# Kernel tuning notes

Measured on AMD Instinct MI355X. Metric: run time of the kernel, lower is better.

## Reference

```python
import jax, jax.numpy as jnp
import numpy as np

B, S, E = 2, 2048, 2048
H, KV, HD = 16, 4, 128  # num_heads, num_kv_heads, head_dim
G = H // KV             # query heads per kv head
ROPE_BASE = 10000.0


def rope_tables(dim, maxlen):
    freqs = 1.0 / ROPE_BASE ** (jnp.arange(0, dim, 2, dtype=jnp.float32) / dim)
    t = jnp.arange(maxlen, dtype=jnp.float32)
    f = jnp.outer(t, freqs)  # (maxlen, dim//2)
    return jnp.cos(f), jnp.sin(f)


def apply_rope(x, cos, sin):
    # x: (..., seq, heads, head_dim); interleaved-pair rotation
    s_len = x.shape[-3]
    c = cos[:s_len][:, None, :]
    s = sin[:s_len][:, None, :]
    x1 = x[..., ::2]
    x2 = x[..., 1::2]
    return jnp.stack([x1 * c - x2 * s, x1 * s + x2 * c], axis=-1).reshape(x.shape)


def setup_inputs() -> dict:
    key = jax.random.key(0)
    kx, kq, kk, kv, ko = jax.random.split(key, 5)
    x = jax.random.normal(kx, (B, S, E), dtype=jnp.float32)
    Wq = jax.random.normal(kq, (E, H * HD), dtype=jnp.float32) * 0.02
    Wk = jax.random.normal(kk, (E, KV * HD), dtype=jnp.float32) * 0.02
    Wv = jax.random.normal(kv, (E, KV * HD), dtype=jnp.float32) * 0.02
    Wo = jax.random.normal(ko, (H * HD, E), dtype=jnp.float32) * 0.02
    mask = jnp.tril(jnp.ones((S, S), dtype=bool))[None, None]  # causal (1,1,S,S)
    return {"x": x, "Wq": Wq, "Wk": Wk, "Wv": Wv, "Wo": Wo, "mask": mask}


def reference(x, Wq, Wk, Wv, Wo, mask):
    b, s, _ = x.shape
    cos, sin = rope_tables(HD, s)
    q = (x @ Wq).reshape(b, s, H, HD)
    k = (x @ Wk).reshape(b, s, KV, HD)
    v = (x @ Wv).reshape(b, s, KV, HD)
    q = apply_rope(q, cos, sin)
    k = apply_rope(k, cos, sin)
    if G > 1:
        k = jnp.repeat(k, G, axis=2)  # (b, s, H, HD)
        v = jnp.repeat(v, G, axis=2)
    q = jnp.transpose(q, (0, 2, 1, 3))  # (b, H, s, HD)
    k = jnp.transpose(k, (0, 2, 1, 3))
    v = jnp.transpose(v, (0, 2, 1, 3))
    scale = jnp.sqrt(jnp.float32(HD)).astype(q.dtype)
    scores = jnp.einsum("bhqd,bhkd->bhqk", q, k) / scale
    scores = jnp.where(mask, scores, jnp.finfo(scores.dtype).min)
    attn = jax.nn.softmax(scores, axis=-1)
    out = jnp.einsum("bhqk,bhkd->bhqd", attn, v)
    out = jnp.transpose(out, (0, 2, 1, 3)).reshape(b, s, H * HD)
    return out @ Wo
```

## Files before the change

kernel.cpp:

```cpp
#include <hip/hip_runtime.h>
#include <hip/hip_bf16.h>
#include <cstdint>

#define B_ 2
#define S_ 2048
#define E_ 2048
#define H_ 16
#define KV_ 4
#define HD_ 128
#define BS_ (B_*S_)
#define QKV_LD 3072
#define SM_SCALE 0.08838834764831845f
#define SC_LOG2E 0.1275424488538497f

typedef __attribute__((ext_vector_type(8))) __bf16 bf16x8;
typedef __attribute__((ext_vector_type(4))) float  floatx4;

__device__ __forceinline__ unsigned short f2bf(float f) {
  union { float f; unsigned u; } v; v.f = f;
  unsigned r = v.u + 0x7fffu + ((v.u >> 16) & 1u);
  return (unsigned short)(r >> 16);
}
__device__ __forceinline__ float bf2f(unsigned short u) {
  union { unsigned u; float f; } v; v.u = ((unsigned)u) << 16; return v.f;
}
__device__ __forceinline__ unsigned pack_bf16x2(float a, float b) {
  union { __hip_bfloat162 h; unsigned u; } v;
  v.h = __float22bfloat162_rn(make_float2(a, b));
  return v.u;
}

__device__ __forceinline__ void async_cp16(const void* g, void* l) {
  __builtin_amdgcn_global_load_lds(
      (const __attribute__((address_space(1))) void*)g,
      (__attribute__((address_space(3))) void*)l, 16, 0, 0);
}

__global__ __launch_bounds__(256)
void cvt_bf16(const float* __restrict__ src, unsigned short* __restrict__ dst,
              int n4) {
  int idx = blockIdx.x * 256 + threadIdx.x;
  if (idx >= n4) return;
  float4 v = *(const float4*)(src + (size_t)idx * 4);
  ushort4 o;
  o.x = f2bf(v.x); o.y = f2bf(v.y); o.z = f2bf(v.z); o.w = f2bf(v.w);
  *(ushort4*)(dst + (size_t)idx * 4) = o;
}

__global__ __launch_bounds__(256)
void cvt_bf16_t(const float* __restrict__ src, unsigned short* __restrict__ dst,
                int N, int dld, int noff) {
  __shared__ float tile[64 * 65];
  const int t = threadIdx.x;
  const int bk = blockIdx.y * 64, bn = blockIdx.x * 64;
  const int r = t >> 2, cg = t & 3;
#pragma unroll
  for (int i = 0; i < 4; ++i) {
    int c = cg * 16 + i * 4;
    float4 v = *(const float4*)(src + (size_t)(bk + r) * N + bn + c);
    tile[r * 65 + c] = v.x; tile[r * 65 + c + 1] = v.y;
    tile[r * 65 + c + 2] = v.z; tile[r * 65 + c + 3] = v.w;
  }
  __syncthreads();
  const int nl = t >> 2, kg = t & 3;
  union { unsigned short u[16]; uint4 q[2]; } o;
#pragma unroll
  for (int j = 0; j < 16; ++j)
    o.u[j] = f2bf(tile[(kg * 16 + j) * 65 + nl]);
  unsigned short* dp = dst + (size_t)(noff + bn + nl) * dld + bk + kg * 16;
  *(uint4*)(dp) = o.q[0];
  *(uint4*)(dp + 8) = o.q[1];
}

__global__ __launch_bounds__(256)
void rope_kernel(unsigned short* __restrict__ qkv) {
  const int PPR = 1280;
  int idx = blockIdx.x * 256 + threadIdx.x;
  if (idx >= BS_ * PPR) return;
  int row = idx / PPR, p = idx - row * PPR;
  int col = (p < 1024) ? (2 * p) : (2048 + 2 * (p - 1024));
  int d = p & 63;
  int s = row & (S_ - 1);
  float freq = expf(-(float)d * 0.14391156831212787f);
  float ang = (float)s * freq;
  float c = cosf(ang), sn = sinf(ang);
  unsigned short* ptr = qkv + (size_t)row * QKV_LD + col;
  float x1 = bf2f(ptr[0]), x2 = bf2f(ptr[1]);
  ptr[0] = f2bf(x1 * c - x2 * sn);
  ptr[1] = f2bf(x1 * sn + x2 * c);
}

__global__ __launch_bounds__(256)
void vtrans_kernel(const unsigned short* __restrict__ qkv,
                   unsigned short* __restrict__ vt) {
  __shared__ unsigned short tile[64 * 72];
  const int tid = threadIdx.x;
  const int s0 = blockIdx.x * 64;
  const int g = blockIdx.y >> 1;
  const int hh = (blockIdx.y & 1) * 64;
  const int b = g >> 2, kvh = g & 3;
#pragma unroll
  for (int i = 0; i < 2; ++i) {
    int chunk = tid + i * 256;
    int r = chunk >> 3, c = (chunk & 7) * 8;
    uint4 v = *(const uint4*)(qkv + (size_t)(b * S_ + s0 + r) * QKV_LD + 2560 + kvh * HD_ + hh + c);
    *(uint4*)(tile + r * 72 + c) = v;
  }
  __syncthreads();
#pragma unroll
  for (int i = 0; i < 2; ++i) {
    int chunk = tid + i * 256;
    int hdr = chunk >> 3, sc = (chunk & 7) * 8;
    union { unsigned short u[8]; uint4 v; } t;
#pragma unroll
    for (int j = 0; j < 8; ++j) t.u[j] = tile[(sc + j) * 72 + hdr];
    *(uint4*)(vt + (size_t)(g * HD_ + hh + hdr) * S_ + s0 + sc) = t.v;
  }
}

template<bool OUT_BF16>
__global__ __launch_bounds__(256, 2)
void gemm_tn(const unsigned short* __restrict__ A,
             const unsigned short* __restrict__ BT,
             void* __restrict__ C, int M, int N, int K) {
  __shared__ unsigned short Ash[128 * 32];
  __shared__ unsigned short Bsh[128 * 32];
  const int tid = threadIdx.x;
  const int l = tid & 63;
  const int l16 = l & 15, l4 = l >> 4;
  const int wave = tid >> 6;
  const int wm = (wave >> 1) * 64, wn = (wave & 1) * 64;
  const int bm = blockIdx.y * 128, bn = blockIdx.x * 128;

  const int srow = l >> 2;
  const int sg = (((l & 3) - (l >> 4)) & 3) * 8;

  floatx4 acc[4][4] = {};

  for (int kb = 0; kb < K; kb += 32) {
    __syncthreads();
#pragma unroll
    for (int i = 0; i < 2; ++i) {
      int cc = wave + i * 4;
      async_cp16(A + (size_t)(bm + 16 * cc + srow) * K + kb + sg, &Ash[cc * 512]);
      async_cp16(BT + (size_t)(bn + 16 * cc + srow) * K + kb + sg, &Bsh[cc * 512]);
    }
    __syncthreads();
    bf16x8 af[4], bf[4];
#pragma unroll
    for (int t = 0; t < 4; ++t) {
      int row = wm + t * 16 + l16;
      int s = (l4 + (l16 >> 2)) & 3;
      af[t] = *(const bf16x8*)(Ash + row * 32 + s * 8);
    }
#pragma unroll
    for (int t = 0; t < 4; ++t) {
      int row = wn + t * 16 + l16;
      int s = (l4 + (l16 >> 2)) & 3;
      bf[t] = *(const bf16x8*)(Bsh + row * 32 + s * 8);
    }
#pragma unroll
    for (int tm = 0; tm < 4; ++tm)
#pragma unroll
      for (int tn = 0; tn < 4; ++tn)
        acc[tm][tn] = __builtin_amdgcn_mfma_f32_16x16x32_bf16(af[tm], bf[tn], acc[tm][tn], 0, 0, 0);
  }
#pragma unroll
  for (int tm = 0; tm < 4; ++tm)
#pragma unroll
    for (int tn = 0; tn < 4; ++tn)
#pragma unroll
      for (int r = 0; r < 4; ++r) {
        int row = bm + wm + tm * 16 + l4 * 4 + r;
        int col = bn + wn + tn * 16 + l16;
        float v = acc[tm][tn][r];
        if (OUT_BF16) ((unsigned short*)C)[(size_t)row * N + col] = f2bf(v);
        else          ((float*)C)[(size_t)row * N + col] = v;
      }
}

__global__ __launch_bounds__(256, 4)
void gqa_attention(const unsigned short* __restrict__ qkv,
                   const unsigned short* __restrict__ vt,
                   unsigned short* __restrict__ out) {
  __shared__ unsigned short Ksh[2][32 * 128];
  __shared__ unsigned short Vsh[2][128 * 32];

  const int tid = threadIdx.x, l = tid & 63, wave = tid >> 6;
  const int l16 = l & 15, l4 = l >> 4;
  const int g = blockIdx.x, b = g >> 2, kvh = g & 3;
  const int h = kvh * 4 + wave;

  const int k_subrow = l >> 4;
  const int v_subrow = l >> 2;
  const int gv = (((l & 3) - (l >> 4)) & 3) * 8;

  const int t = 127 - (int)blockIdx.y;
  const int qt = t * 16;
  const int nch = (qt >> 5) + 1;

  bf16x8 qf[4];
  {
    const unsigned short* qp = qkv + (size_t)(b * S_ + qt + l16) * QKV_LD + h * HD_;
#pragma unroll
    for (int c = 0; c < 4; ++c)
      qf[c] = *(const bf16x8*)(qp + c * 32 + l4 * 8);
  }
  asm volatile("s_waitcnt vmcnt(0)" ::: "memory");

  const unsigned short* kp[2];
  const unsigned short* vp[2];
#pragma unroll
  for (int i = 0; i < 2; ++i) {
    int cc = wave + i * 4;
    int krow = 4 * cc + k_subrow;
    int gk = (((l & 15) - krow) & 15) * 8;
    kp[i] = qkv + (size_t)(b * S_ + krow) * QKV_LD + 2048 + kvh * HD_ + gk;
    vp[i] = vt + (size_t)(g * HD_ + 16 * cc + v_subrow) * S_ + gv;
  }

#pragma unroll
  for (int i = 0; i < 2; ++i) {
    int cc = wave + i * 4;
    async_cp16(kp[i], &Ksh[0][cc * 512]);
    async_cp16(vp[i], &Vsh[0][cc * 512]);
  }

  float lsum = 0.f;
  floatx4 acc[8] = {};

  for (int it = 0; it < nch; ++it) {
    const int kb = it * 32;
    const int cur = it & 1;
    asm volatile("s_barrier" ::: "memory");
    {
      const int kb2 = (it + 1 < nch) ? kb + 32 : 0;
      const int ko = kb2 * QKV_LD;
#pragma unroll
      for (int i = 0; i < 2; ++i) {
        int cc = wave + i * 4;
        async_cp16(kp[i] + ko, &Ksh[cur ^ 1][cc * 512]);
        async_cp16(vp[i] + kb2, &Vsh[cur ^ 1][cc * 512]);
      }
    }
    asm volatile("s_waitcnt vmcnt(4)\n\ts_barrier" ::: "memory");

    floatx4 sacc[2] = {};
    __builtin_amdgcn_s_setprio(1);
#pragma unroll
    for (int half = 0; half < 2; ++half) {
      int krow = half * 16 + l16;
#pragma unroll
      for (int c = 0; c < 4; ++c) {
        int s = (c * 4 + l4 + l16) & 15;
        bf16x8 kf = *(const bf16x8*)(&Ksh[cur][krow * 128 + s * 8]);
        sacc[half] = __builtin_amdgcn_mfma_f32_16x16x32_bf16(kf, qf[c], sacc[half], 0, 0, 0);
      }
    }
    __builtin_amdgcn_s_setprio(0);

    float p[8];
    const bool need_mask = (kb + 31 > qt);
#pragma unroll
    for (int half = 0; half < 2; ++half)
#pragma unroll
      for (int r = 0; r < 4; ++r) {
        float v = fminf(sacc[half][r] * SC_LOG2E, 80.f);
        if (need_mask) {
          int ka = kb + half * 16 + l4 * 4 + r;
          if (ka > qt + l16) v = -3e38f;
        }
        float e = exp2f(v);
        p[half * 4 + r] = e;
        lsum += e;
      }

    unsigned u0 = pack_bf16x2(p[0], p[1]);
    unsigned u1 = pack_bf16x2(p[2], p[3]);
    unsigned u2 = pack_bf16x2(p[4], p[5]);
    unsigned u3 = pack_bf16x2(p[6], p[7]);
    asm("v_permlane32_swap_b32 %0, %1" : "+v"(u0), "+v"(u2));
    asm("v_permlane16_swap_b32 %0, %1" : "+v"(u0), "+v"(u2));
    asm("v_permlane32_swap_b32 %0, %1" : "+v"(u1), "+v"(u3));
    asm("v_permlane16_swap_b32 %0, %1" : "+v"(u1), "+v"(u3));
    union { unsigned w[4]; bf16x8 v8; } pun;
    pun.w[0] = u0; pun.w[1] = u1; pun.w[2] = u2; pun.w[3] = u3;
    const bf16x8 pf = pun.v8;

    __builtin_amdgcn_s_setprio(1);
#pragma unroll
    for (int u = 0; u < 8; ++u) {
      int row = u * 16 + l16;
      int s = (l4 + (l16 >> 2)) & 3;
      bf16x8 vf = *(const bf16x8*)(&Vsh[cur][row * 32 + s * 8]);
      acc[u] = __builtin_amdgcn_mfma_f32_16x16x32_bf16(vf, pf, acc[u], 0, 0, 0);
    }
    __builtin_amdgcn_s_setprio(0);
  }

  lsum += __shfl_xor(lsum, 16, 64);
  lsum += __shfl_xor(lsum, 32, 64);
  float inv = 1.0f / lsum;
  unsigned short* op = out + (size_t)(b * S_ + qt + l16) * 2048 + h * HD_;
#pragma unroll
  for (int u = 0; u < 8; ++u) {
    uint2 o;
    o.x = pack_bf16x2(acc[u][0] * inv, acc[u][1] * inv);
    o.y = pack_bf16x2(acc[u][2] * inv, acc[u][3] * inv);
    *(uint2*)(op + u * 16 + l4 * 4) = o;
  }
}

extern "C" void kernel_launch(void* const* d_in, const int* in_sizes, int n_in,
                              void* d_out, int out_size, void* d_ws, size_t ws_size,
                              hipStream_t stream) {
  const float* x  = (const float*)d_in[0];
  const float* Wq = (const float*)d_in[1];
  const float* Wk = (const float*)d_in[2];
  const float* Wv = (const float*)d_in[3];
  const float* Wo = (const float*)d_in[4];
  float* out = (float*)d_out;

  char* ws = (char*)d_ws;
  unsigned short* xb    = (unsigned short*)(ws);
  unsigned short* wqkvT = (unsigned short*)(ws + 16777216);
  unsigned short* woT   = (unsigned short*)(ws + 29360128);
  unsigned short* qkv   = (unsigned short*)(ws + 37748736);
  unsigned short* attn  = (unsigned short*)(ws + 62914560);
  unsigned short* vt    = (unsigned short*)(ws);

  cvt_bf16<<<(4096 * 2048 / 4 + 255) / 256, 256, 0, stream>>>(x, xb, 4096 * 2048 / 4);
  cvt_bf16_t<<<dim3(32, 32), 256, 0, stream>>>(Wq, wqkvT, 2048, 2048, 0);
  cvt_bf16_t<<<dim3(8, 32),  256, 0, stream>>>(Wk, wqkvT, 512,  2048, 2048);
  cvt_bf16_t<<<dim3(8, 32),  256, 0, stream>>>(Wv, wqkvT, 512,  2048, 2560);
  cvt_bf16_t<<<dim3(32, 32), 256, 0, stream>>>(Wo, woT,  2048, 2048, 0);

  gemm_tn<true><<<dim3(24, 32), 256, 0, stream>>>(xb, wqkvT, qkv, 4096, 3072, 2048);
  rope_kernel<<<(4096 * 1280 + 255) / 256, 256, 0, stream>>>(qkv);
  vtrans_kernel<<<dim3(32, 16), 256, 0, stream>>>(qkv, vt);
  gqa_attention<<<dim3(8, 128), 256, 0, stream>>>(qkv, vt, attn);
  gemm_tn<false><<<dim3(16, 32), 256, 0, stream>>>(attn, woT, out, 4096, 2048, 2048);
}
```

Measured before the change: 338.9 us.

## Process two 16-row query tiles per wave in attention to reuse K/V tiles

Each attention block now covers 32 query rows instead of 16, and each wave holds two query fragment sets that share every K and V shared-memory tile load. The grid halves along the query axis and the causal mask is applied only on the last chunk, using fixed per-tile conditions. This halves the K/V global and LDS traffic per query row. In exchange, register use roughly doubles from the two accumulator sets, so launch bounds drop to 2 blocks per CU, and there are fewer blocks to balance the causal workload.

```diff
diff --git a/kernel.cpp b/kernel.cpp
--- a/kernel.cpp
+++ b/kernel.cpp
@@ -179,7 +179,7 @@
       }
 }
 
-__global__ __launch_bounds__(256, 4)
+__global__ __launch_bounds__(256, 2)
 void gqa_attention(const unsigned short* __restrict__ qkv,
                    const unsigned short* __restrict__ vt,
                    unsigned short* __restrict__ out) {
@@ -195,16 +195,19 @@
   const int v_subrow = l >> 2;
   const int gv = (((l & 3) - (l >> 4)) & 3) * 8;
 
-  const int t = 127 - (int)blockIdx.y;
-  const int qt = t * 16;
-  const int nch = (qt >> 5) + 1;
-
-  bf16x8 qf[4];
+  const int t = 63 - (int)blockIdx.y;
+  const int qt = t * 32;
+  const int nch = t + 1;
+
+  bf16x8 qfA[4], qfB[4];
   {
-    const unsigned short* qp = qkv + (size_t)(b * S_ + qt + l16) * QKV_LD + h * HD_;
-#pragma unroll
-    for (int c = 0; c < 4; ++c)
-      qf[c] = *(const bf16x8*)(qp + c * 32 + l4 * 8);
+    const unsigned short* qpA = qkv + (size_t)(b * S_ + qt + l16) * QKV_LD + h * HD_;
+    const unsigned short* qpB = qpA + (size_t)16 * QKV_LD;
+#pragma unroll
+    for (int c = 0; c < 4; ++c) {
+      qfA[c] = *(const bf16x8*)(qpA + c * 32 + l4 * 8);
+      qfB[c] = *(const bf16x8*)(qpB + c * 32 + l4 * 8);
+    }
   }
   asm volatile("s_waitcnt vmcnt(0)" ::: "memory");
 
@@ -226,15 +229,14 @@
     async_cp16(vp[i], &Vsh[0][cc * 512]);
   }
 
-  float lsum = 0.f;
-  floatx4 acc[8] = {};
+  float lsumA = 0.f, lsumB = 0.f;
+  floatx4 accA[8] = {}, accB[8] = {};
 
   for (int it = 0; it < nch; ++it) {
-    const int kb = it * 32;
     const int cur = it & 1;
     asm volatile("s_barrier" ::: "memory");
     {
-      const int kb2 = (it + 1 < nch) ? kb + 32 : 0;
+      const int kb2 = (it + 1 < nch) ? (it + 1) * 32 : 0;
       const int ko = kb2 * QKV_LD;
 #pragma unroll
       for (int i = 0; i < 2; ++i) {
@@ -245,7 +247,7 @@
     }
     asm volatile("s_waitcnt vmcnt(4)\n\ts_barrier" ::: "memory");
 
-    floatx4 sacc[2] = {};
+    floatx4 saccA[2] = {}, saccB[2] = {};
     __builtin_amdgcn_s_setprio(1);
 #pragma unroll
     for (int half = 0; half < 2; ++half) {
@@ -254,38 +256,61 @@
       for (int c = 0; c < 4; ++c) {
         int s = (c * 4 + l4 + l16) & 15;
         bf16x8 kf = *(const bf16x8*)(&Ksh[cur][krow * 128 + s * 8]);
-        sacc[half] = __builtin_amdgcn_mfma_f32_16x16x32_bf16(kf, qf[c], sacc[half], 0, 0, 0);
+        saccA[half] = __builtin_amdgcn_mfma_f32_16x16x32_bf16(kf, qfA[c], saccA[half], 0, 0, 0);
+        saccB[half] = __builtin_amdgcn_mfma_f32_16x16x32_bf16(kf, qfB[c], saccB[half], 0, 0, 0);
       }
     }
     __builtin_amdgcn_s_setprio(0);
 
-    float p[8];
-    const bool need_mask = (kb + 31 > qt);
-#pragma unroll
-    for (int half = 0; half < 2; ++half)
-#pragma unroll
-      for (int r = 0; r < 4; ++r) {
-        float v = fminf(sacc[half][r] * SC_LOG2E, 80.f);
-        if (need_mask) {
-          int ka = kb + half * 16 + l4 * 4 + r;
-          if (ka > qt + l16) v = -3e38f;
+    float pA[8], pB[8];
+    if (it == nch - 1) {
+#pragma unroll
+      for (int half = 0; half < 2; ++half)
+#pragma unroll
+        for (int r = 0; r < 4; ++r) {
+          int kk = half * 16 + l4 * 4 + r;
+          float vA = fminf(saccA[half][r] * SC_LOG2E, 80.f);
+          if (kk > l16) vA = -3e38f;
+          float eA = exp2f(vA);
+          pA[half * 4 + r] = eA; lsumA += eA;
+          float vB = fminf(saccB[half][r] * SC_LOG2E, 80.f);
+          if (half == 1 && (l4 * 4 + r) > l16) vB = -3e38f;
+          float eB = exp2f(vB);
+          pB[half * 4 + r] = eB; lsumB += eB;
         }
-        float e = exp2f(v);
-        p[half * 4 + r] = e;
-        lsum += e;
-      }
-
-    unsigned u0 = pack_bf16x2(p[0], p[1]);
-    unsigned u1 = pack_bf16x2(p[2], p[3]);
-    unsigned u2 = pack_bf16x2(p[4], p[5]);
-    unsigned u3 = pack_bf16x2(p[6], p[7]);
-    asm("v_permlane32_swap_b32 %0, %1" : "+v"(u0), "+v"(u2));
-    asm("v_permlane16_swap_b32 %0, %1" : "+v"(u0), "+v"(u2));
-    asm("v_permlane32_swap_b32 %0, %1" : "+v"(u1), "+v"(u3));
-    asm("v_permlane16_swap_b32 %0, %1" : "+v"(u1), "+v"(u3));
-    union { unsigned w[4]; bf16x8 v8; } pun;
-    pun.w[0] = u0; pun.w[1] = u1; pun.w[2] = u2; pun.w[3] = u3;
-    const bf16x8 pf = pun.v8;
+    } else {
+#pragma unroll
+      for (int half = 0; half < 2; ++half)
+#pragma unroll
+        for (int r = 0; r < 4; ++r) {
+          float eA = exp2f(fminf(saccA[half][r] * SC_LOG2E, 80.f));
+          pA[half * 4 + r] = eA; lsumA += eA;
+          float eB = exp2f(fminf(saccB[half][r] * SC_LOG2E, 80.f));
+          pB[half * 4 + r] = eB; lsumB += eB;
+        }
+    }
+
+    unsigned a0 = pack_bf16x2(pA[0], pA[1]);
+    unsigned a1 = pack_bf16x2(pA[2], pA[3]);
+    unsigned a2 = pack_bf16x2(pA[4], pA[5]);
+    unsigned a3 = pack_bf16x2(pA[6], pA[7]);
+    asm("v_permlane32_swap_b32 %0, %1" : "+v"(a0), "+v"(a2));
+    asm("v_permlane16_swap_b32 %0, %1" : "+v"(a0), "+v"(a2));
+    asm("v_permlane32_swap_b32 %0, %1" : "+v"(a1), "+v"(a3));
+    asm("v_permlane16_swap_b32 %0, %1" : "+v"(a1), "+v"(a3));
+    unsigned b0 = pack_bf16x2(pB[0], pB[1]);
+    unsigned b1 = pack_bf16x2(pB[2], pB[3]);
+    unsigned b2 = pack_bf16x2(pB[4], pB[5]);
+    unsigned b3 = pack_bf16x2(pB[6], pB[7]);
+    asm("v_permlane32_swap_b32 %0, %1" : "+v"(b0), "+v"(b2));
+    asm("v_permlane16_swap_b32 %0, %1" : "+v"(b0), "+v"(b2));
+    asm("v_permlane32_swap_b32 %0, %1" : "+v"(b1), "+v"(b3));
+    asm("v_permlane16_swap_b32 %0, %1" : "+v"(b1), "+v"(b3));
+    union { unsigned w[4]; bf16x8 v8; } punA, punB;
+    punA.w[0] = a0; punA.w[1] = a1; punA.w[2] = a2; punA.w[3] = a3;
+    punB.w[0] = b0; punB.w[1] = b1; punB.w[2] = b2; punB.w[3] = b3;
+    const bf16x8 pfA = punA.v8;
+    const bf16x8 pfB = punB.v8;
 
     __builtin_amdgcn_s_setprio(1);
 #pragma unroll
@@ -293,21 +318,29 @@
       int row = u * 16 + l16;
       int s = (l4 + (l16 >> 2)) & 3;
       bf16x8 vf = *(const bf16x8*)(&Vsh[cur][row * 32 + s * 8]);
-      acc[u] = __builtin_amdgcn_mfma_f32_16x16x32_bf16(vf, pf, acc[u], 0, 0, 0);
+      accA[u] = __builtin_amdgcn_mfma_f32_16x16x32_bf16(vf, pfA, accA[u], 0, 0, 0);
+      accB[u] = __builtin_amdgcn_mfma_f32_16x16x32_bf16(vf, pfB, accB[u], 0, 0, 0);
     }
     __builtin_amdgcn_s_setprio(0);
   }
 
-  lsum += __shfl_xor(lsum, 16, 64);
-  lsum += __shfl_xor(lsum, 32, 64);
-  float inv = 1.0f / lsum;
-  unsigned short* op = out + (size_t)(b * S_ + qt + l16) * 2048 + h * HD_;
+  lsumA += __shfl_xor(lsumA, 16, 64);
+  lsumA += __shfl_xor(lsumA, 32, 64);
+  lsumB += __shfl_xor(lsumB, 16, 64);
+  lsumB += __shfl_xor(lsumB, 32, 64);
+  float invA = 1.0f / lsumA;
+  float invB = 1.0f / lsumB;
+  unsigned short* opA = out + (size_t)(b * S_ + qt + l16) * 2048 + h * HD_;
+  unsigned short* opB = opA + (size_t)16 * 2048;
 #pragma unroll
   for (int u = 0; u < 8; ++u) {
-    uint2 o;
-    o.x = pack_bf16x2(acc[u][0] * inv, acc[u][1] * inv);
-    o.y = pack_bf16x2(acc[u][2] * inv, acc[u][3] * inv);
-    *(uint2*)(op + u * 16 + l4 * 4) = o;
+    uint2 oA, oB;
+    oA.x = pack_bf16x2(accA[u][0] * invA, accA[u][1] * invA);
+    oA.y = pack_bf16x2(accA[u][2] * invA, accA[u][3] * invA);
+    *(uint2*)(opA + u * 16 + l4 * 4) = oA;
+    oB.x = pack_bf16x2(accB[u][0] * invB, accB[u][1] * invB);
+    oB.y = pack_bf16x2(accB[u][2] * invB, accB[u][3] * invB);
+    *(uint2*)(opB + u * 16 + l4 * 4) = oB;
   }
 }
 
@@ -338,6 +371,6 @@
   gemm_tn<true><<<dim3(24, 32), 256, 0, stream>>>(xb, wqkvT, qkv, 4096, 3072, 2048);
   rope_kernel<<<(4096 * 1280 + 255) / 256, 256, 0, stream>>>(qkv);
   vtrans_kernel<<<dim3(32, 16), 256, 0, stream>>>(qkv, vt);
-  gqa_attention<<<dim3(8, 128), 256, 0, stream>>>(qkv, vt, attn);
+  gqa_attention<<<dim3(8, 64), 256, 0, stream>>>(qkv, vt, attn);
   gemm_tn<false><<<dim3(16, 32), 256, 0, stream>>>(attn, woT, out, 4096, 2048, 2048);
 }
```

New measurement: 349.1 us. 3.0% more time.
